# Kernel optimization log

Measured on AMD Instinct MI355X. Metric: run time of the kernel, lower is better.

## Reference

```python
import jax, jax.numpy as jnp
import numpy as np

N_NODES = 100000
N_EDGES = 1600000
D = 128
NUM_GRAPHS = 256


def setup_inputs() -> dict:
    key = jax.random.key(0)
    ks = jax.random.split(key, 8)
    x = jax.random.normal(ks[0], (N_NODES, D), dtype=jnp.float32)
    edge_index = jax.random.randint(ks[1], (2, N_EDGES), 0, N_NODES, dtype=jnp.int32)
    edge_attr = jax.random.normal(ks[2], (N_EDGES, D), dtype=jnp.float32) * 0.1
    batch = jnp.sort(jax.random.randint(ks[3], (N_NODES,), 0, NUM_GRAPHS, dtype=jnp.int32))
    primary = jax.random.randint(ks[4], (N_NODES,), 0, 2, dtype=jnp.int32)  # 1=primary, 0=condition
    scale = 1.0 / np.sqrt(D)
    W1 = jax.random.normal(ks[5], (D, D), dtype=jnp.float32) * scale
    b1 = jnp.zeros((D,), dtype=jnp.float32)
    W2 = jax.random.normal(ks[6], (D, D), dtype=jnp.float32) * scale
    b2 = jnp.zeros((D,), dtype=jnp.float32)
    return {"x": x, "edge_index": edge_index, "edge_attr": edge_attr,
            "batch": batch, "primary": primary,
            "W1": W1, "b1": b1, "W2": W2, "b2": b2}


def reference(x, edge_index, edge_attr, batch, primary, W1, b1, W2, b2):
    n = x.shape[0]
    # --- GIN-style GNN layer: node_rep = MLP(x + sum_{e:(s->d)} (x[s] + e_attr)) ---
    src, dst = edge_index[0], edge_index[1]
    msg = x[src] + edge_attr                                  # [E, D] gather (memory-bound)
    agg = jax.ops.segment_sum(msg, dst, num_segments=n)       # [N, D] scatter-add
    h = jax.nn.relu((x + agg) @ W1 + b1) @ W2 + b2            # [N, D]

    # --- per-graph mean pool over condition nodes (primary == 0) ---
    cond = (primary == 0)
    condf = cond.astype(h.dtype)[:, None]
    csum = jax.ops.segment_sum(h * condf, batch, num_segments=NUM_GRAPHS)   # [G, D]
    ccnt = jax.ops.segment_sum(condf, batch, num_segments=NUM_GRAPHS)       # [G, 1]
    # graphs with no condition nodes get a zero pool (matches torch branch)
    pool = jnp.where(ccnt > 0, csum / jnp.maximum(ccnt, 1.0), 0.0)          # [G, D]

    # --- assemble rows: per graph, primary rows [h | cond_pool] first, then zero rows
    # for condition nodes (matches the torch concat order) ---
    key = batch * 2 + cond.astype(batch.dtype)      # primary nodes sort before condition nodes
    order = jnp.argsort(key, stable=True)
    h_o = h[order]                                   # [N, D]
    pool_o = pool[batch[order]]                      # [N, D]
    prim_o = (primary[order] == 1)[:, None]
    out = jnp.where(prim_o, jnp.concatenate([h_o, pool_o], axis=1), 0.0)    # [N, 2D]
    return out
```

## Files before the change

kernel.cpp:

```cpp
#include <hip/hip_runtime.h>

#define D 128
#define NG 256

typedef __attribute__((ext_vector_type(8))) short bf16x8;
typedef __attribute__((ext_vector_type(4))) float f32x4;
typedef __attribute__((ext_vector_type(4))) float f4;
typedef __attribute__((ext_vector_type(2))) int i2;
typedef __attribute__((ext_vector_type(4))) ushort u16x4;

__device__ inline ushort f2bf(float f) {
  uint b = __float_as_uint(f);
  return (ushort)((b + 0x7fffu + ((b >> 16) & 1u)) >> 16);
}
__device__ inline float bf2f(ushort u) { return __uint_as_float((uint)u << 16); }

__global__ __launch_bounds__(256) void deg_counts_kernel(const int* __restrict__ ei,
                                                         int* __restrict__ deg,
                                                         const int* __restrict__ batch,
                                                         const int* __restrict__ primary,
                                                         int* __restrict__ ncount,
                                                         int* __restrict__ ccnt, int E, int N) {
  int e = blockIdx.x * blockDim.x + threadIdx.x;
  if (e < E) {
    int d = __builtin_nontemporal_load(&ei[E + e]);
    atomicAdd(&deg[d], 1);
  }
  if (e < N) {
    int g = batch[e];
    atomicAdd(&ncount[g], 1);
    if (primary[e] == 0) atomicAdd(&ccnt[g], 1);
  }
}

__global__ __launch_bounds__(256) void scan_block_sums(const int* __restrict__ deg,
                                                       int* __restrict__ bsum, int N) {
  __shared__ int red[256];
  int t = threadIdx.x;
  int base = blockIdx.x * 1024;
  int s = 0;
#pragma unroll
  for (int j = 0; j < 4; ++j) {
    int i = base + t * 4 + j;
    if (i < N) s += deg[i];
  }
  red[t] = s;
  __syncthreads();
  for (int o = 128; o > 0; o >>= 1) {
    if (t < o) red[t] += red[t + o];
    __syncthreads();
  }
  if (t == 0) bsum[blockIdx.x] = red[0];
}

__global__ void scan_bsum(int* __restrict__ bsum, int nb) {
  if (threadIdx.x == 0) {
    int run = 0;
    for (int i = 0; i < nb; ++i) {
      int v = bsum[i];
      bsum[i] = run;
      run += v;
    }
  }
}

__global__ __launch_bounds__(256) void scan_final(const int* __restrict__ deg,
                                                  const int* __restrict__ bsum,
                                                  int* __restrict__ off, int N) {
  __shared__ int ts[256];
  int t = threadIdx.x;
  int base = blockIdx.x * 1024;
  int v[4];
  int s = 0;
#pragma unroll
  for (int j = 0; j < 4; ++j) {
    int i = base + t * 4 + j;
    v[j] = (i < N) ? deg[i] : 0;
    s += v[j];
  }
  ts[t] = s;
  __syncthreads();
  for (int o = 1; o < 256; o <<= 1) {
    int u = (t >= o) ? ts[t - o] : 0;
    __syncthreads();
    ts[t] += u;
    __syncthreads();
  }
  int excl = ts[t] - s + bsum[blockIdx.x];
#pragma unroll
  for (int j = 0; j < 4; ++j) {
    int i = base + t * 4 + j;
    if (i < N) off[i] = excl;
    excl += v[j];
    if (i == N - 1) off[N] = excl;
  }
}

__global__ __launch_bounds__(256) void fill_kernel(const int* __restrict__ ei,
                                                   const int* __restrict__ off,
                                                   int* __restrict__ cursor,
                                                   i2* __restrict__ csr, int E) {
  int e = blockIdx.x * blockDim.x + threadIdx.x;
  if (e >= E) return;
  int s = __builtin_nontemporal_load(&ei[e]);
  int d = __builtin_nontemporal_load(&ei[E + e]);
  int slot = atomicAdd(&cursor[d], 1);
  i2 v;
  v.x = s;
  v.y = e;
  __builtin_nontemporal_store(v, &csr[off[d] + slot]);
}

__global__ __launch_bounds__(256) void cvt_kernel(const float* __restrict__ x,
                                                  ushort* __restrict__ xb,
                                                  const float* __restrict__ W1,
                                                  const float* __restrict__ W2,
                                                  ushort* __restrict__ W1T,
                                                  ushort* __restrict__ W2T, int total4) {
  int i = blockIdx.x * blockDim.x + threadIdx.x;
  if (i < total4) {
    f4 v = __builtin_nontemporal_load(&((const f4*)x)[i]);
    u16x4 o;
    o.x = f2bf(v.x);
    o.y = f2bf(v.y);
    o.z = f2bf(v.z);
    o.w = f2bf(v.w);
    ((u16x4*)xb)[i] = o;
  }
  if (i < 2 * D * D) {
    int w = i >> 14;
    int k = (i >> 7) & 127;
    int n = i & 127;
    const float* src = w ? W2 : W1;
    ushort* dst = w ? W2T : W1T;
    dst[n * 128 + k] = f2bf(src[k * 128 + n]);
  }
}

__global__ __launch_bounds__(256) void gather_kernel(const ushort* __restrict__ xb,
                                                     const float* __restrict__ ea,
                                                     const i2* __restrict__ csr,
                                                     const int* __restrict__ off,
                                                     ushort* __restrict__ yb, int N) {
  long long tid = (long long)blockIdx.x * blockDim.x + threadIdx.x;
  int n = (int)(tid >> 5);
  int c = (int)(tid & 31);
  if (n >= N) return;
  const f4* ea4 = (const f4*)ea;
  const u16x4* xb4 = (const u16x4*)xb;
  u16x4 self = xb4[(size_t)n * 32 + c];
  f4 acc;
  acc.x = bf2f(self.x);
  acc.y = bf2f(self.y);
  acc.z = bf2f(self.z);
  acc.w = bf2f(self.w);
  int s = off[n], e = off[n + 1];
  int k = s;
  for (; k + 4 <= e; k += 4) {
    i2 p0 = __builtin_nontemporal_load(&csr[k]);
    i2 p1 = __builtin_nontemporal_load(&csr[k + 1]);
    i2 p2 = __builtin_nontemporal_load(&csr[k + 2]);
    i2 p3 = __builtin_nontemporal_load(&csr[k + 3]);
    f4 a0 = __builtin_nontemporal_load(&ea4[(size_t)p0.y * 32 + c]);
    f4 a1 = __builtin_nontemporal_load(&ea4[(size_t)p1.y * 32 + c]);
    f4 a2 = __builtin_nontemporal_load(&ea4[(size_t)p2.y * 32 + c]);
    f4 a3 = __builtin_nontemporal_load(&ea4[(size_t)p3.y * 32 + c]);
    u16x4 u0 = xb4[(size_t)p0.x * 32 + c];
    u16x4 u1 = xb4[(size_t)p1.x * 32 + c];
    u16x4 u2 = xb4[(size_t)p2.x * 32 + c];
    u16x4 u3 = xb4[(size_t)p3.x * 32 + c];
    acc.x += (a0.x + bf2f(u0.x)) + (a1.x + bf2f(u1.x));
    acc.y += (a0.y + bf2f(u0.y)) + (a1.y + bf2f(u1.y));
    acc.z += (a0.z + bf2f(u0.z)) + (a1.z + bf2f(u1.z));
    acc.w += (a0.w + bf2f(u0.w)) + (a1.w + bf2f(u1.w));
    acc.x += (a2.x + bf2f(u2.x)) + (a3.x + bf2f(u3.x));
    acc.y += (a2.y + bf2f(u2.y)) + (a3.y + bf2f(u3.y));
    acc.z += (a2.z + bf2f(u2.z)) + (a3.z + bf2f(u3.z));
    acc.w += (a2.w + bf2f(u2.w)) + (a3.w + bf2f(u3.w));
  }
  for (; k < e; ++k) {
    i2 p0 = __builtin_nontemporal_load(&csr[k]);
    f4 a0 = __builtin_nontemporal_load(&ea4[(size_t)p0.y * 32 + c]);
    u16x4 u0 = xb4[(size_t)p0.x * 32 + c];
    acc.x += a0.x + bf2f(u0.x);
    acc.y += a0.y + bf2f(u0.y);
    acc.z += a0.z + bf2f(u0.z);
    acc.w += a0.w + bf2f(u0.w);
  }
  u16x4 o;
  o.x = f2bf(acc.x);
  o.y = f2bf(acc.y);
  o.z = f2bf(acc.z);
  o.w = f2bf(acc.w);
  __builtin_nontemporal_store(o, &((u16x4*)yb)[(size_t)n * 32 + c]);
}

__global__ void scan_kernel(const int* __restrict__ ncount, int* __restrict__ gstart) {
  __shared__ int a[NG];
  int tx = threadIdx.x;
  int v = ncount[tx];
  a[tx] = v;
  __syncthreads();
  for (int off = 1; off < NG; off <<= 1) {
    int u = (tx >= off) ? a[tx - off] : 0;
    __syncthreads();
    a[tx] += u;
    __syncthreads();
  }
  gstart[tx] = a[tx] - v;
  if (tx == NG - 1) gstart[NG] = a[tx];
}

__global__ __launch_bounds__(256) void rank_kernel(const int* __restrict__ primary,
                                                   const int* __restrict__ gstart,
                                                   const int* __restrict__ ccnt,
                                                   int* __restrict__ pos) {
  int g = blockIdx.x;
  int s = gstart[g], e = gstart[g + 1];
  int pcnt = (e - s) - ccnt[g];
  __shared__ int wcntP[4], wcntC[4];
  int prun = 0, crun = 0;
  for (int i0 = s; i0 < e; i0 += 256) {
    int n = i0 + threadIdx.x;
    bool valid = n < e;
    int isP = (valid && primary[n] == 1) ? 1 : 0;
    int isC = (valid && primary[n] != 1) ? 1 : 0;
    unsigned long long mP = __ballot(isP);
    unsigned long long mC = __ballot(isC);
    int lane = threadIdx.x & 63;
    int wid = threadIdx.x >> 6;
    if (lane == 0) { wcntP[wid] = __popcll(mP); wcntC[wid] = __popcll(mC); }
    __syncthreads();
    int preP = __popcll(mP & ((1ULL << lane) - 1ULL));
    int preC = __popcll(mC & ((1ULL << lane) - 1ULL));
    int woffP = 0, woffC = 0;
#pragma unroll
    for (int ww = 0; ww < 4; ++ww)
      if (ww < wid) { woffP += wcntP[ww]; woffC += wcntC[ww]; }
    int totP = wcntP[0] + wcntP[1] + wcntP[2] + wcntP[3];
    int totC = wcntC[0] + wcntC[1] + wcntC[2] + wcntC[3];
    if (valid) {
      if (isP)
        pos[n] = s + prun + woffP + preP;
      else
        pos[n] = ~(s + pcnt + crun + woffC + preC);
    }
    prun += totP;
    crun += totC;
    __syncthreads();
  }
}

__global__ __launch_bounds__(256) void mlp_mfma_kernel(
    const ushort* __restrict__ yb, float* __restrict__ out,
    const ushort* __restrict__ W1T, const float* __restrict__ b1,
    const ushort* __restrict__ W2T, const float* __restrict__ b2,
    const int* __restrict__ batch, const int* __restrict__ primary,
    const int* __restrict__ pos, float* __restrict__ csum, int N) {
  __shared__ ushort tl[4][16][D];
  __shared__ float csl[4][D];
  const int tid = threadIdx.x;
  const int w = tid >> 6;
  const int l = tid & 63;
  const int lr = l & 15;
  const int lg = l >> 4;
  const int base = blockIdx.x * 64;
  const int m0 = base + w * 16;

  for (int i = tid; i < 4 * D; i += 256) ((float*)csl)[i] = 0.f;
  int gmin = batch[base < N ? base : N - 1];
  __syncthreads();

  f32x4 acc[8];
#pragma unroll
  for (int t = 0; t < 8; ++t) {
    float bv = b1[t * 16 + lr];
    acc[t][0] = bv; acc[t][1] = bv; acc[t][2] = bv; acc[t][3] = bv;
  }
  int arow = m0 + lr;
  if (arow >= N) arow = N - 1;
#pragma unroll
  for (int kk = 0; kk < 4; ++kk) {
    bf16x8 a = *(const bf16x8*)&yb[(size_t)arow * D + kk * 32 + lg * 8];
#pragma unroll
    for (int t = 0; t < 8; ++t) {
      bf16x8 b = *(const bf16x8*)&W1T[(size_t)(t * 16 + lr) * D + kk * 32 + lg * 8];
      acc[t] = __builtin_amdgcn_mfma_f32_16x16x32_bf16(a, b, acc[t], 0, 0, 0);
    }
  }
#pragma unroll
  for (int t = 0; t < 8; ++t) {
#pragma unroll
    for (int r = 0; r < 4; ++r) {
      float v = acc[t][r];
      v = v > 0.f ? v : 0.f;
      int m = lg * 4 + r;
      int col = (t * 16 + lr) ^ ((m & 7) << 3);
      tl[w][m][col] = f2bf(v);
    }
  }
  __syncthreads();

  f32x4 acc2[8];
#pragma unroll
  for (int t = 0; t < 8; ++t) {
    float bv = b2[t * 16 + lr];
    acc2[t][0] = bv; acc2[t][1] = bv; acc2[t][2] = bv; acc2[t][3] = bv;
  }
#pragma unroll
  for (int kk = 0; kk < 4; ++kk) {
    bf16x8 a = *(const bf16x8*)&tl[w][lr][(kk * 32 + lg * 8) ^ ((lr & 7) << 3)];
#pragma unroll
    for (int t = 0; t < 8; ++t) {
      bf16x8 b = *(const bf16x8*)&W2T[(size_t)(t * 16 + lr) * D + kk * 32 + lg * 8];
      acc2[t] = __builtin_amdgcn_mfma_f32_16x16x32_bf16(a, b, acc2[t], 0, 0, 0);
    }
  }

#pragma unroll
  for (int r = 0; r < 4; ++r) {
    int m = m0 + lg * 4 + r;
    if (m >= N) continue;
    int p = pos[m];
    if (p >= 0) {
      size_t ro = (size_t)p * 256;
#pragma unroll
      for (int t = 0; t < 8; ++t)
        __builtin_nontemporal_store(acc2[t][r], &out[ro + t * 16 + lr]);
    } else {
      size_t ro = (size_t)(~p) * 256;
#pragma unroll
      for (int t = 0; t < 8; ++t) {
        __builtin_nontemporal_store(0.0f, &out[ro + t * 16 + lr]);
        __builtin_nontemporal_store(0.0f, &out[ro + 128 + t * 16 + lr]);
      }
      int g = batch[m];
      int gl = g - gmin;
      if (gl < 4) {
#pragma unroll
        for (int t = 0; t < 8; ++t) atomicAdd(&csl[gl][t * 16 + lr], acc2[t][r]);
      } else {
#pragma unroll
        for (int t = 0; t < 8; ++t)
          unsafeAtomicAdd(&csum[(size_t)g * D + t * 16 + lr], acc2[t][r]);
      }
    }
  }
  __syncthreads();
  for (int i = tid; i < 4 * D; i += 256) {
    float v = ((float*)csl)[i];
    if (v != 0.f) {
      int gl = i >> 7, c = i & 127;
      unsafeAtomicAdd(&csum[(size_t)(gmin + gl) * D + c], v);
    }
  }
}

__global__ __launch_bounds__(256) void poolwrite_kernel(const float* __restrict__ csum,
                                                        const int* __restrict__ ccnt,
                                                        const int* __restrict__ batch,
                                                        const int* __restrict__ pos,
                                                        float* __restrict__ out, int N) {
  long long tid = (long long)blockIdx.x * blockDim.x + threadIdx.x;
  int n = (int)(tid >> 5);
  int c = (int)(tid & 31);
  if (n >= N) return;
  int p = pos[n];
  if (p < 0) return;
  int g = batch[n];
  int cnt = ccnt[g];
  f4 v = {0.f, 0.f, 0.f, 0.f};
  if (cnt > 0) {
    f4 s4 = ((const f4*)csum)[(size_t)g * 32 + c];
    float inv = 1.0f / (float)cnt;
    v = s4 * inv;
  }
  __builtin_nontemporal_store(v, &((f4*)out)[(size_t)p * 64 + 32 + c]);
}

extern "C" void kernel_launch(void* const* d_in, const int* in_sizes, int n_in,
                              void* d_out, int out_size, void* d_ws, size_t ws_size,
                              hipStream_t stream) {
  const float* x = (const float*)d_in[0];
  const int* ei = (const int*)d_in[1];
  const float* ea = (const float*)d_in[2];
  const int* batch = (const int*)d_in[3];
  const int* primary = (const int*)d_in[4];
  const float* W1 = (const float*)d_in[5];
  const float* b1 = (const float*)d_in[6];
  const float* W2 = (const float*)d_in[7];
  const float* b2 = (const float*)d_in[8];
  float* out = (float*)d_out;

  const int N = in_sizes[0] / D;
  const int E = in_sizes[1] / 2;
  const int nb = (N + 1023) / 1024;

  float* csum = (float*)d_ws;
  ushort* yb = (ushort*)(csum + (size_t)NG * D);
  ushort* xb = yb + (size_t)N * D;
  ushort* W1T = xb + (size_t)N * D;
  ushort* W2T = W1T + D * D;
  i2* csr = (i2*)(W2T + D * D);
  int* ip = (int*)(csr + (size_t)E);
  int* deg = ip;
  int* off = deg + N;
  int* cursor = off + N + 4;
  int* bsum = cursor + N;
  int* ccnt = bsum + 128;
  int* ncount = ccnt + NG;
  int* gstart = ncount + NG;
  int* pos = gstart + 260;

  hipMemsetAsync(csum, 0, (size_t)NG * D * 4, stream);
  hipMemsetAsync(deg, 0, (size_t)N * 4, stream);
  hipMemsetAsync(cursor, 0, (size_t)N * 4, stream);
  hipMemsetAsync(ccnt, 0, (size_t)NG * 2 * 4, stream);

  deg_counts_kernel<<<(E + 255) / 256, 256, 0, stream>>>(ei, deg, batch, primary, ncount, ccnt,
                                                         E, N);
  scan_block_sums<<<nb, 256, 0, stream>>>(deg, bsum, N);
  scan_bsum<<<1, 64, 0, stream>>>(bsum, nb);
  scan_final<<<nb, 256, 0, stream>>>(deg, bsum, off, N);
  fill_kernel<<<(E + 255) / 256, 256, 0, stream>>>(ei, off, cursor, csr, E);
  cvt_kernel<<<((N * D / 4) + 255) / 256, 256, 0, stream>>>(x, xb, W1, W2, W1T, W2T, N * D / 4);
  {
    long long threads = (long long)N * 32;
    gather_kernel<<<(int)((threads + 255) / 256), 256, 0, stream>>>(xb, ea, csr, off, yb, N);
  }
  scan_kernel<<<1, NG, 0, stream>>>(ncount, gstart);
  rank_kernel<<<NG, 256, 0, stream>>>(primary, gstart, ccnt, pos);
  mlp_mfma_kernel<<<(N + 63) / 64, 256, 0, stream>>>(yb, out, W1T, b1, W2T, b2, batch, primary,
                                                     pos, csum, N);
  poolwrite_kernel<<<(int)(((long long)N * 32 + 255) / 256), 256, 0, stream>>>(csum, ccnt, batch,
                                                                               pos, out, N);
}
```

Before: 648.2 us.

## Fuse edge gather-aggregation into MLP kernel via swizzled LDS tile

Result: faster. 632.3 us (-2.5%).

```diff
diff --git a/kernel.cpp b/kernel.cpp
--- a/kernel.cpp
+++ b/kernel.cpp
@@ -23,7 +23,7 @@
                                                          int* __restrict__ ccnt, int E, int N) {
   int e = blockIdx.x * blockDim.x + threadIdx.x;
   if (e < E) {
-    int d = __builtin_nontemporal_load(&ei[E + e]);
+    int d = ei[E + e];
     atomicAdd(&deg[d], 1);
   }
   if (e < N) {
@@ -102,13 +102,13 @@
                                                    i2* __restrict__ csr, int E) {
   int e = blockIdx.x * blockDim.x + threadIdx.x;
   if (e >= E) return;
-  int s = __builtin_nontemporal_load(&ei[e]);
-  int d = __builtin_nontemporal_load(&ei[E + e]);
+  int s = ei[e];
+  int d = ei[E + e];
   int slot = atomicAdd(&cursor[d], 1);
   i2 v;
   v.x = s;
   v.y = e;
-  __builtin_nontemporal_store(v, &csr[off[d] + slot]);
+  csr[off[d] + slot] = v;
 }
 
 __global__ __launch_bounds__(256) void cvt_kernel(const float* __restrict__ x,
@@ -135,64 +135,6 @@
     ushort* dst = w ? W2T : W1T;
     dst[n * 128 + k] = f2bf(src[k * 128 + n]);
   }
-}
-
-__global__ __launch_bounds__(256) void gather_kernel(const ushort* __restrict__ xb,
-                                                     const float* __restrict__ ea,
-                                                     const i2* __restrict__ csr,
-                                                     const int* __restrict__ off,
-                                                     ushort* __restrict__ yb, int N) {
-  long long tid = (long long)blockIdx.x * blockDim.x + threadIdx.x;
-  int n = (int)(tid >> 5);
-  int c = (int)(tid & 31);
-  if (n >= N) return;
-  const f4* ea4 = (const f4*)ea;
-  const u16x4* xb4 = (const u16x4*)xb;
-  u16x4 self = xb4[(size_t)n * 32 + c];
-  f4 acc;
-  acc.x = bf2f(self.x);
-  acc.y = bf2f(self.y);
-  acc.z = bf2f(self.z);
-  acc.w = bf2f(self.w);
-  int s = off[n], e = off[n + 1];
-  int k = s;
-  for (; k + 4 <= e; k += 4) {
-    i2 p0 = __builtin_nontemporal_load(&csr[k]);
-    i2 p1 = __builtin_nontemporal_load(&csr[k + 1]);
-    i2 p2 = __builtin_nontemporal_load(&csr[k + 2]);
-    i2 p3 = __builtin_nontemporal_load(&csr[k + 3]);
-    f4 a0 = __builtin_nontemporal_load(&ea4[(size_t)p0.y * 32 + c]);
-    f4 a1 = __builtin_nontemporal_load(&ea4[(size_t)p1.y * 32 + c]);
-    f4 a2 = __builtin_nontemporal_load(&ea4[(size_t)p2.y * 32 + c]);
-    f4 a3 = __builtin_nontemporal_load(&ea4[(size_t)p3.y * 32 + c]);
-    u16x4 u0 = xb4[(size_t)p0.x * 32 + c];
-    u16x4 u1 = xb4[(size_t)p1.x * 32 + c];
-    u16x4 u2 = xb4[(size_t)p2.x * 32 + c];
-    u16x4 u3 = xb4[(size_t)p3.x * 32 + c];
-    acc.x += (a0.x + bf2f(u0.x)) + (a1.x + bf2f(u1.x));
-    acc.y += (a0.y + bf2f(u0.y)) + (a1.y + bf2f(u1.y));
-    acc.z += (a0.z + bf2f(u0.z)) + (a1.z + bf2f(u1.z));
-    acc.w += (a0.w + bf2f(u0.w)) + (a1.w + bf2f(u1.w));
-    acc.x += (a2.x + bf2f(u2.x)) + (a3.x + bf2f(u3.x));
-    acc.y += (a2.y + bf2f(u2.y)) + (a3.y + bf2f(u3.y));
-    acc.z += (a2.z + bf2f(u2.z)) + (a3.z + bf2f(u3.z));
-    acc.w += (a2.w + bf2f(u2.w)) + (a3.w + bf2f(u3.w));
-  }
-  for (; k < e; ++k) {
-    i2 p0 = __builtin_nontemporal_load(&csr[k]);
-    f4 a0 = __builtin_nontemporal_load(&ea4[(size_t)p0.y * 32 + c]);
-    u16x4 u0 = xb4[(size_t)p0.x * 32 + c];
-    acc.x += a0.x + bf2f(u0.x);
-    acc.y += a0.y + bf2f(u0.y);
-    acc.z += a0.z + bf2f(u0.z);
-    acc.w += a0.w + bf2f(u0.w);
-  }
-  u16x4 o;
-  o.x = f2bf(acc.x);
-  o.y = f2bf(acc.y);
-  o.z = f2bf(acc.z);
-  o.w = f2bf(acc.w);
-  __builtin_nontemporal_store(o, &((u16x4*)yb)[(size_t)n * 32 + c]);
 }
 
 __global__ void scan_kernel(const int* __restrict__ ncount, int* __restrict__ gstart) {
@@ -251,25 +193,86 @@
   }
 }
 
-__global__ __launch_bounds__(256) void mlp_mfma_kernel(
-    const ushort* __restrict__ yb, float* __restrict__ out,
+__global__ __launch_bounds__(256, 4) void fused_gather_mlp_kernel(
+    const ushort* __restrict__ xb, const float* __restrict__ ea,
+    const i2* __restrict__ csr, const int* __restrict__ off, float* __restrict__ out,
     const ushort* __restrict__ W1T, const float* __restrict__ b1,
     const ushort* __restrict__ W2T, const float* __restrict__ b2,
     const int* __restrict__ batch, const int* __restrict__ primary,
     const int* __restrict__ pos, float* __restrict__ csum, int N) {
+  __shared__ ushort ylds[64][D];
   __shared__ ushort tl[4][16][D];
   __shared__ float csl[4][D];
   const int tid = threadIdx.x;
+  const int base = blockIdx.x * 64;
+
+  for (int i = tid; i < 4 * D; i += 256) ((float*)csl)[i] = 0.f;
+  const int gmin = batch[base < N ? base : N - 1];
+
+  {
+    const int gid = tid >> 5;
+    const int c = tid & 31;
+    const f4* ea4 = (const f4*)ea;
+    const u16x4* xb4 = (const u16x4*)xb;
+    for (int i = 0; i < 8; ++i) {
+      const int m = gid * 8 + i;
+      const int n = base + m;
+      f4 acc = {0.f, 0.f, 0.f, 0.f};
+      if (n < N) {
+        u16x4 self = xb4[(size_t)n * 32 + c];
+        acc.x = bf2f(self.x);
+        acc.y = bf2f(self.y);
+        acc.z = bf2f(self.z);
+        acc.w = bf2f(self.w);
+        int s = off[n], e = off[n + 1];
+        int k = s;
+        for (; k + 4 <= e; k += 4) {
+          i2 p0 = csr[k];
+          i2 p1 = csr[k + 1];
+          i2 p2 = csr[k + 2];
+          i2 p3 = csr[k + 3];
+          f4 a0 = __builtin_nontemporal_load(&ea4[(size_t)p0.y * 32 + c]);
+          f4 a1 = __builtin_nontemporal_load(&ea4[(size_t)p1.y * 32 + c]);
+          f4 a2 = __builtin_nontemporal_load(&ea4[(size_t)p2.y * 32 + c]);
+          f4 a3 = __builtin_nontemporal_load(&ea4[(size_t)p3.y * 32 + c]);
+          u16x4 u0 = xb4[(size_t)p0.x * 32 + c];
+          u16x4 u1 = xb4[(size_t)p1.x * 32 + c];
+          u16x4 u2 = xb4[(size_t)p2.x * 32 + c];
+          u16x4 u3 = xb4[(size_t)p3.x * 32 + c];
+          acc.x += (a0.x + bf2f(u0.x)) + (a1.x + bf2f(u1.x));
+          acc.y += (a0.y + bf2f(u0.y)) + (a1.y + bf2f(u1.y));
+          acc.z += (a0.z + bf2f(u0.z)) + (a1.z + bf2f(u1.z));
+          acc.w += (a0.w + bf2f(u0.w)) + (a1.w + bf2f(u1.w));
+          acc.x += (a2.x + bf2f(u2.x)) + (a3.x + bf2f(u3.x));
+          acc.y += (a2.y + bf2f(u2.y)) + (a3.y + bf2f(u3.y));
+          acc.z += (a2.z + bf2f(u2.z)) + (a3.z + bf2f(u3.z));
+          acc.w += (a2.w + bf2f(u2.w)) + (a3.w + bf2f(u3.w));
+        }
+        for (; k < e; ++k) {
+          i2 p0 = csr[k];
+          f4 a0 = __builtin_nontemporal_load(&ea4[(size_t)p0.y * 32 + c]);
+          u16x4 u0 = xb4[(size_t)p0.x * 32 + c];
+          acc.x += a0.x + bf2f(u0.x);
+          acc.y += a0.y + bf2f(u0.y);
+          acc.z += a0.z + bf2f(u0.z);
+          acc.w += a0.w + bf2f(u0.w);
+        }
+      }
+      u16x4 o;
+      o.x = f2bf(acc.x);
+      o.y = f2bf(acc.y);
+      o.z = f2bf(acc.z);
+      o.w = f2bf(acc.w);
+      *(u16x4*)((char*)&ylds[m][0] + ((c * 8) ^ (i << 4))) = o;
+    }
+  }
+  __syncthreads();
+
   const int w = tid >> 6;
   const int l = tid & 63;
   const int lr = l & 15;
   const int lg = l >> 4;
-  const int base = blockIdx.x * 64;
   const int m0 = base + w * 16;
-
-  for (int i = tid; i < 4 * D; i += 256) ((float*)csl)[i] = 0.f;
-  int gmin = batch[base < N ? base : N - 1];
-  __syncthreads();
 
   f32x4 acc[8];
 #pragma unroll
@@ -277,11 +280,11 @@
     float bv = b1[t * 16 + lr];
     acc[t][0] = bv; acc[t][1] = bv; acc[t][2] = bv; acc[t][3] = bv;
   }
-  int arow = m0 + lr;
-  if (arow >= N) arow = N - 1;
+  const char* arow_base = (const char*)&ylds[w * 16 + lr][0];
+  const int arow_swz = (lr & 7) << 4;
 #pragma unroll
   for (int kk = 0; kk < 4; ++kk) {
-    bf16x8 a = *(const bf16x8*)&yb[(size_t)arow * D + kk * 32 + lg * 8];
+    bf16x8 a = *(const bf16x8*)(arow_base + ((kk * 64 + lg * 16) ^ arow_swz));
 #pragma unroll
     for (int t = 0; t < 8; ++t) {
       bf16x8 b = *(const bf16x8*)&W1T[(size_t)(t * 16 + lr) * D + kk * 32 + lg * 8];
@@ -397,8 +400,7 @@
   const int nb = (N + 1023) / 1024;
 
   float* csum = (float*)d_ws;
-  ushort* yb = (ushort*)(csum + (size_t)NG * D);
-  ushort* xb = yb + (size_t)N * D;
+  ushort* xb = (ushort*)(csum + (size_t)NG * D);
   ushort* W1T = xb + (size_t)N * D;
   ushort* W2T = W1T + D * D;
   i2* csr = (i2*)(W2T + D * D);
@@ -424,14 +426,11 @@
   scan_final<<<nb, 256, 0, stream>>>(deg, bsum, off, N);
   fill_kernel<<<(E + 255) / 256, 256, 0, stream>>>(ei, off, cursor, csr, E);
   cvt_kernel<<<((N * D / 4) + 255) / 256, 256, 0, stream>>>(x, xb, W1, W2, W1T, W2T, N * D / 4);
-  {
-    long long threads = (long long)N * 32;
-    gather_kernel<<<(int)((threads + 255) / 256), 256, 0, stream>>>(xb, ea, csr, off, yb, N);
-  }
   scan_kernel<<<1, NG, 0, stream>>>(ncount, gstart);
   rank_kernel<<<NG, 256, 0, stream>>>(primary, gstart, ccnt, pos);
-  mlp_mfma_kernel<<<(N + 63) / 64, 256, 0, stream>>>(yb, out, W1T, b1, W2T, b2, batch, primary,
-                                                     pos, csum, N);
+  fused_gather_mlp_kernel<<<(N + 63) / 64, 256, 0, stream>>>(xb, ea, csr, off, out, W1T, b1,
+                                                             W2T, b2, batch, primary, pos,
+                                                             csum, N);
   poolwrite_kernel<<<(int)(((long long)N * 32 + 255) / 256), 256, 0, stream>>>(csum, ccnt, batch,
                                                                                pos, out, N);
 }
```
